# Performance work log

Hardware: AMD Instinct MI355X
Metric: run time of the kernel (lower is better)

The kernel has to match this reference:

```python
import jax, jax.numpy as jnp
import numpy as np

NEG = -1e9
TAU = 1.0
N_SAMPLES = 5
SWEEP = (0.1, 0.5, 5)


def layer_norm(x, g, b, eps=1e-5):
    m = x.mean(-1, keepdims=True)
    v = x.var(-1, keepdims=True)
    return (x - m) / jnp.sqrt(v + eps) * g + b


def entmax15(z):
    # exact 1.5-entmax along last axis (Peters & Martins 2019 sort-based algorithm)
    z = z / 2.0
    zs = jnp.sort(z, axis=-1)[..., ::-1]               # descending
    T = z.shape[-1]
    kk = jnp.arange(1, T + 1, dtype=z.dtype)
    mean = jnp.cumsum(zs, -1) / kk
    mean_sq = jnp.cumsum(zs * zs, -1) / kk
    ss = kk * (mean_sq - mean * mean)
    delta = jnp.clip((1.0 - ss) / kk, 0.0)
    tau = mean - jnp.sqrt(delta)
    support = jnp.sum((tau <= zs).astype(jnp.int32), -1, keepdims=True)  # k_star
    tau_star = jnp.take_along_axis(tau, support - 1, axis=-1)
    return jnp.square(jnp.clip(z - tau_star, 0.0))


def stochastic_topk(key, scores, attn, k, tau, n_samples):
    # vectorized over samples AND batch rows with per-row variable k:
    # threshold = k-th largest perturbed score per row (ties measure-zero w/ gumbel)
    u = jax.random.uniform(key, (n_samples,) + scores.shape)
    noise = -jnp.log(-jnp.log(u + 1e-6) + 1e-6)
    pert = jnp.where(attn[None] == 0, NEG, scores[None] + noise * tau)  # [S,B,T]
    srt = jnp.sort(pert, -1)[..., ::-1]
    idx = jnp.broadcast_to((k - 1)[None, :, None], pert.shape[:2] + (1,))
    thr = jnp.take_along_axis(srt, idx, axis=-1)       # [S,B,1]
    h = (pert >= thr).astype(scores.dtype)
    return h.mean(0)                                   # [B,T]


def pool(tok, attn):
    # masked mean pooling (stand-in for sent_encoder.pool)
    return (tok * attn[..., None]).sum(1) / jnp.clip(attn.sum(1, keepdims=True), 1e-6)


def _forward(ids, embeddings, attn, ln_g, ln_b, W1, b1, W2, b2, emb_table):
    emb = embeddings * attn[..., None]
    h = jax.nn.gelu(layer_norm(emb, ln_g, ln_b) @ W1 + b1, approximate=False)
    scores = (h @ W2 + b2)[..., 0]                     # [B,T]
    scores = jnp.where(attn == 0, NEG, scores)

    tok = emb_table[ids]                               # stand-in token embeddings
    full_rep = jax.lax.stop_gradient(pool(tok, attn))  # torch.no_grad path

    T_eff = attn.sum(1)                                # [B]
    # g_soft is identical across the rho sweep in the original; hoisted here
    g_soft = entmax15(scores / TAU) * attn
    g_soft = g_soft / jnp.clip(g_soft.sum(1, keepdims=True), 1e-6)

    key = jax.random.key(42)
    rhos = np.linspace(*SWEEP)
    g_sweep, loss_sweep, rho_eff_sweep = [], [], []
    recon_sum = jnp.zeros((), embeddings.dtype)
    g = None
    for j, rho in enumerate(rhos):
        k = jnp.maximum((float(rho) * T_eff).astype(jnp.int32), 1)
        g_hard = stochastic_topk(jax.random.fold_in(key, j), scores, attn, k, TAU, N_SAMPLES)
        # straight-through: hard forward, soft (entmax) backward
        g = jax.lax.stop_gradient(g_hard) - jax.lax.stop_gradient(g_soft) + g_soft
        rho_eff_sweep.append(g.sum(1) / T_eff)
        eff_attn = attn * g
        pred_rep = pool(tok, eff_attn)
        l_r = jnp.mean(jnp.square(pred_rep - full_rep))  # recon_loss = MSE stand-in
        recon_sum = recon_sum + l_r
        g_sweep.append(g)
        loss_sweep.append(l_r)
    recon_avg = recon_sum / len(rhos)
    return g, jnp.stack(g_sweep), recon_avg, jnp.stack(loss_sweep), jnp.stack(rho_eff_sweep)


def setup_inputs() -> dict:
    key = jax.random.key(0)
    B, T, D, H, V = 8, 2048, 1024, 1365, 32000
    ks = jax.random.split(key, 8)
    return {
        "ids": jax.random.randint(ks[0], (B, T), 0, V),
        "embeddings": jax.random.normal(ks[1], (B, T, D), jnp.float32),
        "attn": jnp.ones((B, T), jnp.float32),
        "ln_g": jnp.ones((D,), jnp.float32),
        "ln_b": jnp.zeros((D,), jnp.float32),
        "W1": jax.random.normal(ks[2], (D, H), jnp.float32) * 0.02,
        "b1": jnp.zeros((H,), jnp.float32),
        "W2": jax.random.normal(ks[3], (H, 1), jnp.float32) * 0.02,
        "b2": jnp.zeros((1,), jnp.float32),
        "emb_table": jax.random.normal(ks[4], (V, D), jnp.float32) * 0.02,
    }


def reference(ids, embeddings, attn, ln_g, ln_b, W1, b1, W2, b2, emb_table):
    return _forward(ids, embeddings, attn, ln_g, ln_b, W1, b1, W2, b2, emb_table)
```

## Files before the change

kernel.cpp:

```cpp
#include <hip/hip_runtime.h>
#include <math.h>
#include <stdint.h>

#define B_ 8
#define T_ 2048
#define D_ 1024
#define H_ 1365
#define HPAD 1408
#define NTOK (B_*T_)
#define NSAMP 5
#define NRHO 5

typedef float  f32x4  __attribute__((ext_vector_type(4)));
typedef __bf16 bf16x8 __attribute__((ext_vector_type(8)));

#define WS_SCORES 0
#define WS_CNT    (WS_SCORES + NTOK*8)
#define WS_PREDW  (WS_CNT + NRHO*B_*T_*4)
#define WS_FULLW  (WS_PREDW + NRHO*B_*D_*8)
#define WS_SUMEFF (WS_FULLW + B_*D_*8)
#define WS_SUMATT (WS_SUMEFF + NRHO*B_*8)
#define WS_SUMG   (WS_SUMATT + B_*8)
#define WS_ZERO_BYTES (WS_SUMG + NRHO*B_*8)
#define WS_STATS  (WS_SUMG + NRHO*B_*8)
#define WS_W1THI  (WS_STATS + NTOK*8)
#define WS_W1TLO  (WS_W1THI + (size_t)HPAD*D_*2)
#define WS_AHI    (WS_W1TLO + (size_t)HPAD*D_*2)
#define WS_ALO    (WS_AHI + (size_t)NTOK*D_*2)
#define WS_FULL_END (WS_ALO + (size_t)NTOK*D_*2)

#define OUT_G      0
#define OUT_GSW    16384
#define OUT_RECON  98304
#define OUT_LOSS   98305
#define OUT_RHOEFF 98310

__device__ inline unsigned short f2bf(float x) {
    uint32_t u = __float_as_uint(x);
    return (unsigned short)((u + 0x7FFFu + ((u >> 16) & 1u)) >> 16);
}

__launch_bounds__(256)
__global__ void k_w1t(const float* __restrict__ W1, unsigned short* __restrict__ hi,
                      unsigned short* __restrict__ lo)
{
    __shared__ float tile[32][33];
    const int tid = threadIdx.x;
    const int bk = blockIdx.x & 31;
    const int bh = blockIdx.x >> 5;
    const int k0 = bk * 32, h0 = bh * 32;
    const int a = tid & 31, b = tid >> 5;
    #pragma unroll
    for (int i = 0; i < 4; ++i) {
        int k = k0 + b + i * 8;
        int h = h0 + a;
        tile[b + i*8][a] = (h < H_) ? W1[(size_t)k * H_ + h] : 0.0f;
    }
    __syncthreads();
    #pragma unroll
    for (int i = 0; i < 4; ++i) {
        int hrow = h0 + b + i * 8;
        int kcol = k0 + a;
        float v = tile[a][b + i*8];
        unsigned short hb = f2bf(v);
        float hf = __uint_as_float((uint32_t)hb << 16);
        unsigned short lb = f2bf(v - hf);
        size_t dst = (size_t)hrow * D_ + kcol;
        hi[dst] = hb; lo[dst] = lb;
    }
}

__launch_bounds__(256)
__global__ void k_asplit(const float* __restrict__ emb, const float* __restrict__ attn,
                         const float* __restrict__ ln_g, const float* __restrict__ ln_b,
                         unsigned short* __restrict__ ahi, unsigned short* __restrict__ alo)
{
    const int tid = threadIdx.x, l = tid & 63, w = tid >> 6;
    const int t0 = blockIdx.x * 64;
    for (int tk = w; tk < 64; tk += 4) {
        const int tg = t0 + tk;
        const float av = attn[tg];
        const float* row = emb + (size_t)tg * D_;
        float rv[16];
        double s1 = 0.0, s2 = 0.0;
        #pragma unroll
        for (int i = 0; i < 16; ++i) {
            rv[i] = row[i*64 + l];
            double x = (double)rv[i] * (double)av;
            s1 += x; s2 += x * x;
        }
        for (int m = 32; m; m >>= 1) { s1 += __shfl_xor(s1, m); s2 += __shfl_xor(s2, m); }
        double mean = s1 / (double)D_;
        double var  = s2 / (double)D_ - mean * mean;
        double inv  = 1.0 / sqrt(var + 1e-5);
        float sc  = (float)((double)av * inv);
        float nsh = -(float)(mean * inv);
        #pragma unroll
        for (int i = 0; i < 16; ++i) {
            int k = i * 64 + l;
            float t  = fmaf(rv[i], sc, nsh);
            float xn = fmaf(t, ln_g[k], ln_b[k]);
            unsigned short hb = f2bf(xn);
            float hf = __uint_as_float((uint32_t)hb << 16);
            size_t dst = (size_t)tg * D_ + k;
            ahi[dst] = hb;
            alo[dst] = f2bf(xn - hf);
        }
    }
}

__launch_bounds__(256)
__global__ void k_stats(const float* __restrict__ emb, const float* __restrict__ attn,
                        float2* __restrict__ stats)
{
    const int tid = threadIdx.x, l = tid & 63, w = tid >> 6;
    const int t0 = blockIdx.x * 64;
    for (int tk = w; tk < 64; tk += 4) {
        const int tg = t0 + tk;
        const float av = attn[tg];
        const float* row = emb + (size_t)tg * D_;
        double s1 = 0.0, s2 = 0.0;
        #pragma unroll
        for (int i = 0; i < D_/64; ++i) {
            double x = (double)row[i*64 + l] * (double)av;
            s1 += x; s2 += x * x;
        }
        for (int m = 32; m; m >>= 1) { s1 += __shfl_xor(s1, m); s2 += __shfl_xor(s2, m); }
        if (l == 0) {
            double mean = s1 / (double)D_;
            double var  = s2 / (double)D_ - mean * mean;
            double inv  = 1.0 / sqrt(var + 1e-5);
            stats[tg] = make_float2((float)((double)av * inv), (float)(mean * inv));
        }
    }
}

__launch_bounds__(256)
__global__ void k_scores(const unsigned short* __restrict__ ahi,
                         const unsigned short* __restrict__ alo,
                         const unsigned short* __restrict__ w1thi,
                         const unsigned short* __restrict__ w1tlo,
                         const float* __restrict__ b1, const float* __restrict__ W2,
                         double* __restrict__ scores)
{
    __shared__ __align__(16) unsigned short sAhi[128*40];
    __shared__ __align__(16) unsigned short sAlo[128*40];
    __shared__ __align__(16) unsigned short sBhi[128*40];
    __shared__ __align__(16) unsigned short sBlo[128*40];

    const int tid = threadIdx.x;
    const int blk = blockIdx.x;
    const int xcd = blk & 7, slot = blk >> 3;
    const int lin = xcd * 176 + slot;
    const int tt = lin / 11, hh = lin - tt * 11;
    const int t0 = tt * 128;
    const int h0 = hh * 128;

    f32x4 acc[4][4];
    #pragma unroll
    for (int r = 0; r < 4; ++r)
        #pragma unroll
        for (int c = 0; c < 4; ++c) acc[r][c] = (f32x4){0.f, 0.f, 0.f, 0.f};

    const int l = tid & 63, w = tid >> 6;
    const int lm = l & 15, lq = l >> 4;
    const int wr = (w >> 1) * 64;
    const int wc = (w & 1) * 64;

    const int row = tid >> 2, oct = tid & 3;
    const int dstoff  = row * 40 + oct * 8;
    const int dstoff2 = (64 + row) * 40 + oct * 8;

    for (int kc = 0; kc < D_; kc += 32) {
        size_t srcA  = (size_t)(t0 + row) * D_ + kc + oct * 8;
        size_t srcA2 = srcA + (size_t)64 * D_;
        size_t srcB  = (size_t)(h0 + row) * D_ + kc + oct * 8;
        size_t srcB2 = srcB + (size_t)64 * D_;
        *(bf16x8*)&sAhi[dstoff]  = *(const bf16x8*)&ahi[srcA];
        *(bf16x8*)&sAlo[dstoff]  = *(const bf16x8*)&alo[srcA];
        *(bf16x8*)&sAhi[dstoff2] = *(const bf16x8*)&ahi[srcA2];
        *(bf16x8*)&sAlo[dstoff2] = *(const bf16x8*)&alo[srcA2];
        *(bf16x8*)&sBhi[dstoff]  = *(const bf16x8*)&w1thi[srcB];
        *(bf16x8*)&sBlo[dstoff]  = *(const bf16x8*)&w1tlo[srcB];
        *(bf16x8*)&sBhi[dstoff2] = *(const bf16x8*)&w1thi[srcB2];
        *(bf16x8*)&sBlo[dstoff2] = *(const bf16x8*)&w1tlo[srcB2];
        __syncthreads();
        bf16x8 ah[4], al[4], bh[4], bl[4];
        #pragma unroll
        for (int r = 0; r < 4; ++r) {
            int off = (wr + r * 16 + lm) * 40 + lq * 8;
            ah[r] = *(const bf16x8*)&sAhi[off];
            al[r] = *(const bf16x8*)&sAlo[off];
        }
        #pragma unroll
        for (int c = 0; c < 4; ++c) {
            int off = (wc + c * 16 + lm) * 40 + lq * 8;
            bh[c] = *(const bf16x8*)&sBhi[off];
            bl[c] = *(const bf16x8*)&sBlo[off];
        }
        #pragma unroll
        for (int r = 0; r < 4; ++r)
            #pragma unroll
            for (int c = 0; c < 4; ++c) {
                acc[r][c] = __builtin_amdgcn_mfma_f32_16x16x32_bf16(ah[r], bh[c], acc[r][c], 0, 0, 0);
                acc[r][c] = __builtin_amdgcn_mfma_f32_16x16x32_bf16(ah[r], bl[c], acc[r][c], 0, 0, 0);
                acc[r][c] = __builtin_amdgcn_mfma_f32_16x16x32_bf16(al[r], bh[c], acc[r][c], 0, 0, 0);
            }
        __syncthreads();
    }

    float b1v[4], w2v[4];
    #pragma unroll
    for (int c = 0; c < 4; ++c) {
        int hg = h0 + wc + c * 16 + lm;
        bool ok = (hg < H_);
        b1v[c] = ok ? b1[hg] : 0.0f;
        w2v[c] = ok ? W2[hg] : 0.0f;
    }
    const float is2 = 0.70710678118654752440f;
    #pragma unroll
    for (int r = 0; r < 4; ++r) {
        #pragma unroll
        for (int i = 0; i < 4; ++i) {
            float ps = 0.0f;
            #pragma unroll
            for (int c = 0; c < 4; ++c) {
                float z  = acc[r][c][i] + b1v[c];
                float gl = 0.5f * z * (1.0f + erff(z * is2));
                ps = fmaf(gl, w2v[c], ps);
            }
            double psd = (double)ps;
            psd += __shfl_xor(psd, 1);
            psd += __shfl_xor(psd, 2);
            psd += __shfl_xor(psd, 4);
            psd += __shfl_xor(psd, 8);
            if (lm == 0)
                atomicAdd(&scores[t0 + wr + r * 16 + lq * 4 + i], psd);
        }
    }
}

__launch_bounds__(256)
__global__ void k_scores_fb(const float* __restrict__ emb, const float* __restrict__ ln_g,
                            const float* __restrict__ ln_b, const float2* __restrict__ stats,
                            const unsigned short* __restrict__ w1thi,
                            const unsigned short* __restrict__ w1tlo,
                            const float* __restrict__ b1, const float* __restrict__ W2,
                            double* __restrict__ scores)
{
    __shared__ __align__(16) unsigned short sAhi[128*40];
    __shared__ __align__(16) unsigned short sAlo[128*40];
    __shared__ __align__(16) unsigned short sBhi[128*40];
    __shared__ __align__(16) unsigned short sBlo[128*40];
    __shared__ float sS1[128], sS2[128];

    const int tid = threadIdx.x;
    const int blk = blockIdx.x;
    const int xcd = blk & 7, slot = blk >> 3;
    const int lin = xcd * 176 + slot;
    const int tt = lin / 11, hh = lin - tt * 11;
    const int t0 = tt * 128;
    const int h0 = hh * 128;

    if (tid < 128) {
        float2 st = stats[t0 + tid];
        sS1[tid] = st.x; sS2[tid] = st.y;
    }
    f32x4 acc[4][4];
    #pragma unroll
    for (int r = 0; r < 4; ++r)
        #pragma unroll
        for (int c = 0; c < 4; ++c) acc[r][c] = (f32x4){0.f, 0.f, 0.f, 0.f};
    const int l = tid & 63, w = tid >> 6;
    const int lm = l & 15, lq = l >> 4;
    const int wr = (w >> 1) * 64;
    const int wc = (w & 1) * 64;
    __syncthreads();

    for (int kc = 0; kc < D_; kc += 32) {
        #pragma unroll
        for (int r2 = 0; r2 < 2; ++r2) {
            int g = tid + r2 * 256;
            int row = g >> 2, oct = g & 3;
            size_t src = (size_t)(h0 + row) * D_ + kc + oct * 8;
            int dst = row * 40 + oct * 8;
            *(bf16x8*)&sBhi[dst] = *(const bf16x8*)&w1thi[src];
            *(bf16x8*)&sBlo[dst] = *(const bf16x8*)&w1tlo[src];
        }
        #pragma unroll
        for (int r2 = 0; r2 < 2; ++r2) {
            int g = tid + r2 * 256;
            int tk = g >> 2, oct = g & 3;
            int tg = t0 + tk, dg = kc + oct * 8;
            const float* ep = emb + (size_t)tg * D_ + dg;
            float s1 = sS1[tk], ns2 = -sS2[tk];
            union { unsigned short s[8]; bf16x8 v; } hi, lo;
            #pragma unroll
            for (int j = 0; j < 8; ++j) {
                float t  = fmaf(ep[j], s1, ns2);
                float xn = fmaf(t, ln_g[dg + j], ln_b[dg + j]);
                unsigned short hb = f2bf(xn);
                float hf = __uint_as_float((uint32_t)hb << 16);
                hi.s[j] = hb;
                lo.s[j] = f2bf(xn - hf);
            }
            int dst = tk * 40 + oct * 8;
            *(bf16x8*)&sAhi[dst] = hi.v;
            *(bf16x8*)&sAlo[dst] = lo.v;
        }
        __syncthreads();
        bf16x8 ah[4], al[4], bh[4], bl[4];
        #pragma unroll
        for (int r = 0; r < 4; ++r) {
            int off = (wr + r * 16 + lm) * 40 + lq * 8;
            ah[r] = *(const bf16x8*)&sAhi[off];
            al[r] = *(const bf16x8*)&sAlo[off];
        }
        #pragma unroll
        for (int c = 0; c < 4; ++c) {
            int off = (wc + c * 16 + lm) * 40 + lq * 8;
            bh[c] = *(const bf16x8*)&sBhi[off];
            bl[c] = *(const bf16x8*)&sBlo[off];
        }
        #pragma unroll
        for (int r = 0; r < 4; ++r)
            #pragma unroll
            for (int c = 0; c < 4; ++c) {
                acc[r][c] = __builtin_amdgcn_mfma_f32_16x16x32_bf16(ah[r], bh[c], acc[r][c], 0, 0, 0);
                acc[r][c] = __builtin_amdgcn_mfma_f32_16x16x32_bf16(ah[r], bl[c], acc[r][c], 0, 0, 0);
                acc[r][c] = __builtin_amdgcn_mfma_f32_16x16x32_bf16(al[r], bh[c], acc[r][c], 0, 0, 0);
            }
        __syncthreads();
    }
    float b1v[4], w2v[4];
    #pragma unroll
    for (int c = 0; c < 4; ++c) {
        int hg = h0 + wc + c * 16 + lm;
        bool ok = (hg < H_);
        b1v[c] = ok ? b1[hg] : 0.0f;
        w2v[c] = ok ? W2[hg] : 0.0f;
    }
    const float is2 = 0.70710678118654752440f;
    #pragma unroll
    for (int r = 0; r < 4; ++r) {
        #pragma unroll
        for (int i = 0; i < 4; ++i) {
            float ps = 0.0f;
            #pragma unroll
            for (int c = 0; c < 4; ++c) {
                float z  = acc[r][c][i] + b1v[c];
                float gl = 0.5f * z * (1.0f + erff(z * is2));
                ps = fmaf(gl, w2v[c], ps);
            }
            double psd = (double)ps;
            psd += __shfl_xor(psd, 1);
            psd += __shfl_xor(psd, 2);
            psd += __shfl_xor(psd, 4);
            psd += __shfl_xor(psd, 8);
            if (lm == 0)
                atomicAdd(&scores[t0 + wr + r * 16 + lq * 4 + i], psd);
        }
    }
}

__device__ inline void tf2x32(uint32_t k0, uint32_t k1, uint32_t x0, uint32_t x1,
                              uint32_t& o0, uint32_t& o1)
{
    const uint32_t ks2 = k0 ^ k1 ^ 0x1BD11BDAu;
    x0 += k0; x1 += k1;
#define ROT_(v,d) (((v) << (d)) | ((v) >> (32 - (d))))
#define RND_(R) { x0 += x1; x1 = ROT_(x1, R); x1 ^= x0; }
    RND_(13) RND_(15) RND_(26) RND_(6)
    x0 += k1;  x1 += ks2 + 1u;
    RND_(17) RND_(29) RND_(16) RND_(24)
    x0 += ks2; x1 += k0 + 2u;
    RND_(13) RND_(15) RND_(26) RND_(6)
    x0 += k0;  x1 += k1 + 3u;
    RND_(17) RND_(29) RND_(16) RND_(24)
    x0 += k1;  x1 += ks2 + 4u;
    RND_(13) RND_(15) RND_(26) RND_(6)
    x0 += ks2; x1 += k0 + 5u;
    o0 = x0; o1 = x1;
#undef RND_
#undef ROT_
}

__launch_bounds__(256)
__global__ void k_topk(const double* __restrict__ scores, const float* __restrict__ attn,
                       const float* __restrict__ b2, int* __restrict__ cnt)
{
    __shared__ unsigned long long keys[2048];
    __shared__ unsigned int hist[256];
    __shared__ unsigned int wsum[4];
    __shared__ unsigned int selDigit, selBase;
    __shared__ double red[4];

    const int tid = threadIdx.x;
    const int blk = blockIdx.x;
    const int j = blk / 40;
    const int s = (blk % 40) >> 3;
    const int b = blk & 7;

    uint32_t kk0, kk1;
    tf2x32(0u, 42u, 0u, (uint32_t)j, kk0, kk1);

    double tsum = 0.0;
    for (int t = tid; t < T_; t += 256) tsum += (double)attn[b * T_ + t];
    for (int m = 32; m; m >>= 1) tsum += __shfl_xor(tsum, m);
    if ((tid & 63) == 0) red[tid >> 6] = tsum;
    __syncthreads();
    const double Teff = red[0] + red[1] + red[2] + red[3];
    const float rhos[5] = {0.1f, 0.2f, 0.3f, 0.4f, 0.5f};
    int kst = (int)(rhos[j] * (float)Teff);
    if (kst < 1) kst = 1;

    const double bb2 = (double)b2[0];
    #pragma unroll
    for (int r = 0; r < 8; ++r) {
        int t = tid + r * 256;
        int f = (s * 8 + b) * T_ + t;
        uint32_t o0, o1;
        tf2x32(kk0, kk1, 0u, (uint32_t)f, o0, o1);
        uint32_t bits = o0 ^ o1;
        float u = __uint_as_float((bits >> 9) | 0x3f800000u) - 1.0f;
        float a1 = (float)((double)u + (double)1e-6f);
        float la = (float)log((double)a1);
        float m1 = (float)((double)1e-6f - (double)la);
        float lb = (float)log((double)m1);
        float noise = -lb;
        float av = attn[b * T_ + t];
        double pv = (av == 0.0f) ? -1e9 : (scores[b * T_ + t] + bb2 + (double)noise);
        unsigned long long uu = (unsigned long long)__double_as_longlong(pv);
        keys[t] = (uu >> 63) ? ~uu : (uu | 0x8000000000000000ull);
    }
    __syncthreads();

    unsigned long long pfx = 0;
    unsigned int plo = (unsigned int)(2048 - kst);
    const int lane = tid & 63, wv = tid >> 6;
    for (int pass = 0; pass < 8; ++pass) {
        const int shift = 56 - 8 * pass;
        const unsigned long long maskhi = (pass == 0) ? 0ull : (~0ull << (64 - 8 * pass));
        hist[tid] = 0;
        __syncthreads();
        #pragma unroll
        for (int r = 0; r < 8; ++r) {
            unsigned long long kk = keys[tid + r * 256];
            if ((kk & maskhi) == pfx)
                atomicAdd(&hist[(unsigned int)((kk >> shift) & 255ull)], 1u);
        }
        __syncthreads();
        unsigned int own = hist[tid];
        int val = (int)own;
        #pragma unroll
        for (int off = 1; off < 64; off <<= 1) {
            int n = __shfl_up(val, off);
            if (lane >= off) val += n;
        }
        if (lane == 63) wsum[wv] = (unsigned int)val;
        __syncthreads();
        unsigned int woff = 0;
        for (int q = 0; q < wv; ++q) woff += wsum[q];
        unsigned int incl = (unsigned int)val + woff;
        unsigned int excl = incl - own;
        if (own > 0 && plo >= excl && plo < incl) { selDigit = (unsigned int)tid; selBase = excl; }
        __syncthreads();
        pfx |= ((unsigned long long)selDigit << shift);
        plo -= selBase;
        __syncthreads();
    }

    #pragma unroll
    for (int r = 0; r < 8; ++r) {
        int t = tid + r * 256;
        if (keys[t] >= pfx) atomicAdd(&cnt[(j * 8 + b) * T_ + t], 1);
    }
}

__launch_bounds__(256)
__global__ void k_gfin(const int* __restrict__ cnt, const float* __restrict__ attn,
                       float* __restrict__ out, double* __restrict__ sumeff,
                       double* __restrict__ sumatt, double* __restrict__ sumg)
{
    __shared__ double redA[4], redB[4], redC[4];
    const int j = blockIdx.x >> 3, b = blockIdx.x & 7;
    const int tid = threadIdx.x;
    double sg = 0.0, se = 0.0, sa = 0.0;
    for (int t = tid; t < T_; t += 256) {
        int c = cnt[(j * 8 + b) * T_ + t];
        float g  = (float)c / 5.0f;
        float av = attn[b * T_ + t];
        out[OUT_GSW + (j * 8 + b) * T_ + t] = g;
        if (j == 4) out[OUT_G + b * T_ + t] = g;
        sg += (double)g;
        se += (double)(av * g);
        sa += (double)av;
    }
    for (int m = 32; m; m >>= 1) { sg += __shfl_xor(sg, m); se += __shfl_xor(se, m); sa += __shfl_xor(sa, m); }
    if ((tid & 63) == 0) { redA[tid>>6] = sg; redB[tid>>6] = se; redC[tid>>6] = sa; }
    __syncthreads();
    if (tid == 0) {
        sg = redA[0]+redA[1]+redA[2]+redA[3];
        se = redB[0]+redB[1]+redB[2]+redB[3];
        sa = redC[0]+redC[1]+redC[2]+redC[3];
        sumg[j*8+b] = sg; sumeff[j*8+b] = se;
        if (j == 0) sumatt[b] = sa;
        out[OUT_RHOEFF + j*8 + b] = (float)sg / (float)sa;
    }
}

__launch_bounds__(256)
__global__ void k_pool(const int* __restrict__ ids, const float* __restrict__ attn,
                       const float* __restrict__ out, const float* __restrict__ emb_table,
                       double* __restrict__ predw, double* __restrict__ fullw)
{
    __shared__ int   sid[128];
    __shared__ float sw[6][128];
    const int blk = blockIdx.x;
    const int b  = blk >> 6;
    const int dc = (blk >> 4) & 3;
    const int tc = blk & 15;
    const int tid = threadIdx.x;
    const int d = dc * 256 + tid;
    if (tid < 128) {
        int t = tc * 128 + tid;
        sid[tid] = ids[b * T_ + t];
        float av = attn[b * T_ + t];
        sw[0][tid] = av;
        #pragma unroll
        for (int j = 0; j < 5; ++j) {
            float g = out[OUT_GSW + (j * 8 + b) * T_ + t];
            sw[1 + j][tid] = av * g;
        }
    }
    __syncthreads();
    double acc[6] = {0,0,0,0,0,0};
    for (int i = 0; i < 128; ++i) {
        float val = emb_table[(size_t)sid[i] * D_ + d];
        #pragma unroll
        for (int c = 0; c < 6; ++c) acc[c] += (double)(val * sw[c][i]);
    }
    atomicAdd(&fullw[b * D_ + d], acc[0]);
    #pragma unroll
    for (int j = 0; j < 5; ++j)
        atomicAdd(&predw[(j * 8 + b) * D_ + d], acc[1 + j]);
}

__launch_bounds__(256)
__global__ void k_loss(const double* __restrict__ predw, const double* __restrict__ fullw,
                       const double* __restrict__ sumeff, const double* __restrict__ sumatt,
                       float* __restrict__ out)
{
    __shared__ double red[4];
    __shared__ float lr[5];
    const int tid = threadIdx.x;
    for (int j = 0; j < 5; ++j) {
        double p = 0.0;
        for (int i = tid; i < B_ * D_; i += 256) {
            int b = i >> 10;
            double dF = sumatt[b];        if (dF < 1e-6) dF = 1e-6;
            double dE = sumeff[j*8 + b];  if (dE < 1e-6) dE = 1e-6;
            double diff = predw[j * B_ * D_ + i] / dE - fullw[i] / dF;
            p += diff * diff;
        }
        for (int m = 32; m; m >>= 1) p += __shfl_xor(p, m);
        if ((tid & 63) == 0) red[tid >> 6] = p;
        __syncthreads();
        if (tid == 0) {
            double t = red[0] + red[1] + red[2] + red[3];
            lr[j] = (float)(t / (double)(B_ * D_));
            out[OUT_LOSS + j] = lr[j];
        }
        __syncthreads();
    }
    if (tid == 0) {
        float srec = 0.0f;
        for (int j = 0; j < 5; ++j) srec += lr[j];
        out[OUT_RECON] = srec / 5.0f;
    }
}

extern "C" void kernel_launch(void* const* d_in, const int* in_sizes, int n_in,
                              void* d_out, int out_size, void* d_ws, size_t ws_size,
                              hipStream_t stream)
{
    const int*   ids  = (const int*)  d_in[0];
    const float* emb  = (const float*)d_in[1];
    const float* attn = (const float*)d_in[2];
    const float* ln_g = (const float*)d_in[3];
    const float* ln_b = (const float*)d_in[4];
    const float* W1   = (const float*)d_in[5];
    const float* b1   = (const float*)d_in[6];
    const float* W2   = (const float*)d_in[7];
    const float* b2   = (const float*)d_in[8];
    const float* et   = (const float*)d_in[9];
    float* out = (float*)d_out;
    char*  ws  = (char*)d_ws;

    double* scores = (double*)(ws + WS_SCORES);
    int*    cnt    = (int*)   (ws + WS_CNT);
    double* predw  = (double*)(ws + WS_PREDW);
    double* fullw  = (double*)(ws + WS_FULLW);
    double* sumeff = (double*)(ws + WS_SUMEFF);
    double* sumatt = (double*)(ws + WS_SUMATT);
    double* sumg   = (double*)(ws + WS_SUMG);
    float2* stats  = (float2*)(ws + WS_STATS);
    unsigned short* w1thi = (unsigned short*)(ws + WS_W1THI);
    unsigned short* w1tlo = (unsigned short*)(ws + WS_W1TLO);
    unsigned short* ahi   = (unsigned short*)(ws + WS_AHI);
    unsigned short* alo   = (unsigned short*)(ws + WS_ALO);

    hipMemsetAsync(d_ws, 0, WS_ZERO_BYTES, stream);

    k_w1t<<<44*32, 256, 0, stream>>>(W1, w1thi, w1tlo);
    if (ws_size >= WS_FULL_END) {
        k_asplit<<<NTOK/64, 256, 0, stream>>>(emb, attn, ln_g, ln_b, ahi, alo);
        k_scores<<<1408, 256, 0, stream>>>(ahi, alo, w1thi, w1tlo, b1, W2, scores);
    } else {
        k_stats<<<NTOK/64, 256, 0, stream>>>(emb, attn, stats);
        k_scores_fb<<<1408, 256, 0, stream>>>(emb, ln_g, ln_b, stats, w1thi, w1tlo,
                                              b1, W2, scores);
    }
    k_topk<<<NRHO * NSAMP * B_, 256, 0, stream>>>(scores, attn, b2, cnt);
    k_gfin<<<NRHO * B_, 256, 0, stream>>>(cnt, attn, out, sumeff, sumatt, sumg);
    k_pool<<<512, 256, 0, stream>>>(ids, attn, out, et, predw, fullw);
    k_loss<<<1, 256, 0, stream>>>(predw, fullw, sumeff, sumatt, out);
}
```

Baseline: 525.8 us.

## Rewrite scores GEMM with 8-wave 128x256 tiles and triple-buffered direct-to-LDS loads

```diff
diff --git a/kernel.cpp b/kernel.cpp
--- a/kernel.cpp
+++ b/kernel.cpp
@@ -6,7 +6,7 @@
 #define T_ 2048
 #define D_ 1024
 #define H_ 1365
-#define HPAD 1408
+#define HPAD 1536
 #define NTOK (B_*T_)
 #define NSAMP 5
 #define NRHO 5
@@ -135,26 +135,57 @@
     }
 }
 
-__launch_bounds__(256)
-__global__ void k_scores(const unsigned short* __restrict__ ahi,
-                         const unsigned short* __restrict__ alo,
-                         const unsigned short* __restrict__ w1thi,
-                         const unsigned short* __restrict__ w1tlo,
-                         const float* __restrict__ b1, const float* __restrict__ W2,
-                         double* __restrict__ scores)
-{
-    __shared__ __align__(16) unsigned short sAhi[128*40];
-    __shared__ __align__(16) unsigned short sAlo[128*40];
-    __shared__ __align__(16) unsigned short sBhi[128*40];
-    __shared__ __align__(16) unsigned short sBlo[128*40];
+#define BUFU 24576
+#define OFF_ALO 4096
+#define OFF_BHI 8192
+#define OFF_BLO 16384
+#define KSTEPS 32
+
+__device__ __forceinline__ void gll16(const unsigned short* g, unsigned short* l)
+{
+    __builtin_amdgcn_global_load_lds((const __attribute__((address_space(1))) void*)g,
+                                     (__attribute__((address_space(3))) void*)l, 16, 0, 0);
+}
+
+__launch_bounds__(512, 2)
+__global__ void k_scores8(const unsigned short* __restrict__ ahi,
+                          const unsigned short* __restrict__ alo,
+                          const unsigned short* __restrict__ w1thi,
+                          const unsigned short* __restrict__ w1tlo,
+                          const float* __restrict__ b1, const float* __restrict__ W2,
+                          double* __restrict__ scores)
+{
+    __shared__ __align__(16) unsigned short smem[3*BUFU];
 
     const int tid = threadIdx.x;
     const int blk = blockIdx.x;
-    const int xcd = blk & 7, slot = blk >> 3;
-    const int lin = xcd * 176 + slot;
-    const int tt = lin / 11, hh = lin - tt * 11;
-    const int t0 = tt * 128;
-    const int h0 = hh * 128;
+    const int lin = (blk & 7) * 96 + (blk >> 3);
+    const int mm = lin / 6, hh = lin - mm * 6;
+    const int t0 = mm * 128;
+    const int h0 = hh * 256;
+
+    const int l  = tid & 63, w = tid >> 6;
+    const int wr = w >> 2, wcn = w & 3;
+    const int lm = l & 15, lq = l >> 4;
+
+    const int lrow  = l >> 2;
+    const int lslot = (l & 3) ^ ((l >> 3) & 3);
+    const unsigned short* sA_hi  = ahi   + (size_t)(t0 + w*16 + lrow) * D_ + lslot*8;
+    const unsigned short* sA_lo  = alo   + (size_t)(t0 + w*16 + lrow) * D_ + lslot*8;
+    const unsigned short* sB_hi0 = w1thi + (size_t)(h0 + w*32 + lrow) * D_ + lslot*8;
+    const unsigned short* sB_hi1 = sB_hi0 + 16*D_;
+    const unsigned short* sB_lo0 = w1tlo + (size_t)(h0 + w*32 + lrow) * D_ + lslot*8;
+    const unsigned short* sB_lo1 = sB_lo0 + 16*D_;
+    const int dAhi  = w*512,            dAlo  = OFF_ALO + w*512;
+    const int dBhi0 = OFF_BHI + w*1024, dBhi1 = dBhi0 + 512;
+    const int dBlo0 = OFF_BLO + w*1024, dBlo1 = dBlo0 + 512;
+
+    const int sw8 = (lq ^ ((lm >> 1) & 3)) * 8;
+    int offAh[4], offBh[4];
+    #pragma unroll
+    for (int r = 0; r < 4; ++r) offAh[r] = (wr*64 + r*16 + lm)*32 + sw8;
+    #pragma unroll
+    for (int c = 0; c < 4; ++c) offBh[c] = OFF_BHI + (wcn*64 + c*16 + lm)*32 + sw8;
 
     f32x4 acc[4][4];
     #pragma unroll
@@ -162,57 +193,86 @@
         #pragma unroll
         for (int c = 0; c < 4; ++c) acc[r][c] = (f32x4){0.f, 0.f, 0.f, 0.f};
 
-    const int l = tid & 63, w = tid >> 6;
-    const int lm = l & 15, lq = l >> 4;
-    const int wr = (w >> 1) * 64;
-    const int wc = (w & 1) * 64;
-
-    const int row = tid >> 2, oct = tid & 3;
-    const int dstoff  = row * 40 + oct * 8;
-    const int dstoff2 = (64 + row) * 40 + oct * 8;
-
-    for (int kc = 0; kc < D_; kc += 32) {
-        size_t srcA  = (size_t)(t0 + row) * D_ + kc + oct * 8;
-        size_t srcA2 = srcA + (size_t)64 * D_;
-        size_t srcB  = (size_t)(h0 + row) * D_ + kc + oct * 8;
-        size_t srcB2 = srcB + (size_t)64 * D_;
-        *(bf16x8*)&sAhi[dstoff]  = *(const bf16x8*)&ahi[srcA];
-        *(bf16x8*)&sAlo[dstoff]  = *(const bf16x8*)&alo[srcA];
-        *(bf16x8*)&sAhi[dstoff2] = *(const bf16x8*)&ahi[srcA2];
-        *(bf16x8*)&sAlo[dstoff2] = *(const bf16x8*)&alo[srcA2];
-        *(bf16x8*)&sBhi[dstoff]  = *(const bf16x8*)&w1thi[srcB];
-        *(bf16x8*)&sBlo[dstoff]  = *(const bf16x8*)&w1tlo[srcB];
-        *(bf16x8*)&sBhi[dstoff2] = *(const bf16x8*)&w1thi[srcB2];
-        *(bf16x8*)&sBlo[dstoff2] = *(const bf16x8*)&w1tlo[srcB2];
-        __syncthreads();
-        bf16x8 ah[4], al[4], bh[4], bl[4];
-        #pragma unroll
-        for (int r = 0; r < 4; ++r) {
-            int off = (wr + r * 16 + lm) * 40 + lq * 8;
-            ah[r] = *(const bf16x8*)&sAhi[off];
-            al[r] = *(const bf16x8*)&sAlo[off];
-        }
-        #pragma unroll
-        for (int c = 0; c < 4; ++c) {
-            int off = (wc + c * 16 + lm) * 40 + lq * 8;
-            bh[c] = *(const bf16x8*)&sBhi[off];
-            bl[c] = *(const bf16x8*)&sBlo[off];
-        }
+    gll16(sA_hi,       &smem[0*BUFU + dAhi]);
+    gll16(sA_lo,       &smem[0*BUFU + dAlo]);
+    gll16(sB_hi0,      &smem[0*BUFU + dBhi0]);
+    gll16(sB_hi1,      &smem[0*BUFU + dBhi1]);
+    gll16(sB_lo0,      &smem[0*BUFU + dBlo0]);
+    gll16(sB_lo1,      &smem[0*BUFU + dBlo1]);
+    gll16(sA_hi  + 32, &smem[1*BUFU + dAhi]);
+    gll16(sA_lo  + 32, &smem[1*BUFU + dAlo]);
+    gll16(sB_hi0 + 32, &smem[1*BUFU + dBhi0]);
+    gll16(sB_hi1 + 32, &smem[1*BUFU + dBhi1]);
+    gll16(sB_lo0 + 32, &smem[1*BUFU + dBlo0]);
+    gll16(sB_lo1 + 32, &smem[1*BUFU + dBlo1]);
+    asm volatile("s_waitcnt vmcnt(6)" ::: "memory");
+    asm volatile("s_barrier" ::: "memory");
+
+    int dbase = 0, ebase = 2*BUFU;
+    #pragma unroll 1
+    for (int t = 0; t < KSTEPS; ++t) {
+        const int  stK = (t + 2) * 32;
+        const bool st  = (t < KSTEPS - 2);
+        bf16x8 ah[4], bh[4];
+        #pragma unroll
+        for (int r = 0; r < 4; ++r) ah[r] = *(const bf16x8*)&smem[dbase + offAh[r]];
+        #pragma unroll
+        for (int c = 0; c < 4; ++c) bh[c] = *(const bf16x8*)&smem[dbase + offBh[c]];
+        if (st) { gll16(sA_hi + stK, &smem[ebase + dAhi]);
+                  gll16(sA_lo + stK, &smem[ebase + dAlo]); }
+        asm volatile("s_barrier" ::: "memory");
+        asm volatile("s_waitcnt lgkmcnt(0)" ::: "memory");
+        __builtin_amdgcn_sched_barrier(0);
+        __builtin_amdgcn_s_setprio(1);
         #pragma unroll
         for (int r = 0; r < 4; ++r)
             #pragma unroll
-            for (int c = 0; c < 4; ++c) {
+            for (int c = 0; c < 4; ++c)
                 acc[r][c] = __builtin_amdgcn_mfma_f32_16x16x32_bf16(ah[r], bh[c], acc[r][c], 0, 0, 0);
+        __builtin_amdgcn_s_setprio(0);
+        asm volatile("s_barrier" ::: "memory");
+        bf16x8 bl[4];
+        #pragma unroll
+        for (int c = 0; c < 4; ++c) bl[c] = *(const bf16x8*)&smem[dbase + offBh[c] + (OFF_BLO - OFF_BHI)];
+        if (st) { gll16(sB_hi0 + stK, &smem[ebase + dBhi0]);
+                  gll16(sB_hi1 + stK, &smem[ebase + dBhi1]); }
+        asm volatile("s_barrier" ::: "memory");
+        asm volatile("s_waitcnt lgkmcnt(0)" ::: "memory");
+        __builtin_amdgcn_sched_barrier(0);
+        __builtin_amdgcn_s_setprio(1);
+        #pragma unroll
+        for (int r = 0; r < 4; ++r)
+            #pragma unroll
+            for (int c = 0; c < 4; ++c)
                 acc[r][c] = __builtin_amdgcn_mfma_f32_16x16x32_bf16(ah[r], bl[c], acc[r][c], 0, 0, 0);
+        __builtin_amdgcn_s_setprio(0);
+        asm volatile("s_barrier" ::: "memory");
+        bf16x8 al[4];
+        #pragma unroll
+        for (int r = 0; r < 4; ++r) al[r] = *(const bf16x8*)&smem[dbase + offAh[r] + OFF_ALO];
+        if (st) { gll16(sB_lo0 + stK, &smem[ebase + dBlo0]);
+                  gll16(sB_lo1 + stK, &smem[ebase + dBlo1]); }
+        asm volatile("s_barrier" ::: "memory");
+        asm volatile("s_waitcnt lgkmcnt(0)" ::: "memory");
+        __builtin_amdgcn_sched_barrier(0);
+        __builtin_amdgcn_s_setprio(1);
+        #pragma unroll
+        for (int r = 0; r < 4; ++r)
+            #pragma unroll
+            for (int c = 0; c < 4; ++c)
                 acc[r][c] = __builtin_amdgcn_mfma_f32_16x16x32_bf16(al[r], bh[c], acc[r][c], 0, 0, 0);
-            }
-        __syncthreads();
+        __builtin_amdgcn_s_setprio(0);
+        if (st) asm volatile("s_waitcnt vmcnt(6)" ::: "memory");
+        else    asm volatile("s_waitcnt vmcnt(0)" ::: "memory");
+        asm volatile("s_barrier" ::: "memory");
+        dbase = (dbase == 2*BUFU) ? 0 : dbase + BUFU;
+        ebase = (ebase == 2*BUFU) ? 0 : ebase + BUFU;
     }
 
     float b1v[4], w2v[4];
     #pragma unroll
     for (int c = 0; c < 4; ++c) {
-        int hg = h0 + wc + c * 16 + lm;
+        int hg = h0 + wcn*64 + c*16 + lm;
         bool ok = (hg < H_);
         b1v[c] = ok ? b1[hg] : 0.0f;
         w2v[c] = ok ? W2[hg] : 0.0f;
@@ -235,7 +295,7 @@
             psd += __shfl_xor(psd, 4);
             psd += __shfl_xor(psd, 8);
             if (lm == 0)
-                atomicAdd(&scores[t0 + wr + r * 16 + lq * 4 + i], psd);
+                atomicAdd(&scores[t0 + wr*64 + r*16 + lq*4 + i], psd);
         }
     }
 }
@@ -612,10 +672,10 @@
 
     hipMemsetAsync(d_ws, 0, WS_ZERO_BYTES, stream);
 
-    k_w1t<<<44*32, 256, 0, stream>>>(W1, w1thi, w1tlo);
+    k_w1t<<<48*32, 256, 0, stream>>>(W1, w1thi, w1tlo);
     if (ws_size >= WS_FULL_END) {
         k_asplit<<<NTOK/64, 256, 0, stream>>>(emb, attn, ln_g, ln_b, ahi, alo);
-        k_scores<<<1408, 256, 0, stream>>>(ahi, alo, w1thi, w1tlo, b1, W2, scores);
+        k_scores8<<<768, 512, 0, stream>>>(ahi, alo, w1thi, w1tlo, b1, W2, scores);
     } else {
         k_stats<<<NTOK/64, 256, 0, stream>>>(emb, attn, stats);
         k_scores_fb<<<1408, 256, 0, stream>>>(emb, ln_g, ln_b, stats, w1thi, w1tlo,
```

Result: faster. 502.0 us (-4.5%).
